# Kernel tuning notes

Measured on AMD Instinct MI355X. Metric: run time of the kernel, lower is better.

## Reference

```python
import jax, jax.numpy as jnp
import numpy as np

B, C, H, W = 2, 72, 96, 96
FACTOR = 4  # input_dim // output_dim = 72 // 18


def setup_inputs() -> dict:
    key = jax.random.key(0)
    ks = jax.random.split(key, 7)
    s = 1.0 / np.sqrt(C)
    return {
        "x": jax.random.normal(ks[0], (B, C, H, W), dtype=jnp.float32),
        "Wq": jax.random.normal(ks[1], (C, C), dtype=jnp.float32) * s,
        "bq": jax.random.normal(ks[2], (C,), dtype=jnp.float32) * 0.01,
        "Wk": jax.random.normal(ks[3], (C, C), dtype=jnp.float32) * s,
        "bk": jax.random.normal(ks[4], (C,), dtype=jnp.float32) * 0.01,
        "Wv": jax.random.normal(ks[5], (C, C), dtype=jnp.float32) * s,
        "bv": jax.random.normal(ks[6], (C,), dtype=jnp.float32) * 0.01,
    }


def reference(x, Wq, bq, Wk, bk, Wv, bv):
    b, c, h, w = x.shape
    n = h * w
    flat = x.reshape(b, c, n)  # [B, C, N]
    # 1x1 convs == per-pixel channel matmuls
    q = jnp.einsum('dc,bcn->bdn', Wq, flat) + bq[None, :, None]
    k = jnp.einsum('dc,bcn->bdn', Wk, flat) + bk[None, :, None]
    v = jnp.einsum('dc,bcn->bdn', Wv, flat) + bv[None, :, None]
    # scores[b,i,j] = sum_c q[b,c,i] * k[b,c,j]  (no 1/sqrt(d) scaling, as in source)
    scores = jnp.einsum('bci,bcj->bij', q, k)  # [B, N, N]
    attn = jax.nn.softmax(scores, axis=-1)
    # weighted_values = bmm(v, attn^T): wv[b,c,i] = sum_j v[b,c,j] * attn[b,i,j]
    wv = jnp.einsum('bcj,bij->bci', v, attn)  # [B, C, N]
    wv = wv.reshape(b, c // FACTOR, FACTOR, h, w)
    xg = x.reshape(b, c // FACTOR, FACTOR, h, w)
    pooled = jnp.sum(xg * wv, axis=2)  # [B, C//FACTOR, H, W]
    return pooled
```

## Files before the change

kernel.cpp:

```cpp
#include <hip/hip_runtime.h>

#define NPIX 9216
#define CIN 72
#define CP 96
#define SPLITS 8
#define JCHUNK (NPIX / SPLITS)
#define JTILES (JCHUNK / 64)
#define L2E   1.44269504088896f
#define EXPB  46.1662413084468f

typedef __attribute__((ext_vector_type(8))) short bf16x8;
typedef __attribute__((ext_vector_type(8))) _Float16 f16x8;
typedef __attribute__((ext_vector_type(4))) float f32x4;

#define MFMA_BF16(A,B,C) __builtin_amdgcn_mfma_f32_16x16x32_bf16(A,B,C,0,0,0)
#define MFMA_F16(A,B,C)  __builtin_amdgcn_mfma_f32_16x16x32_f16(A,B,C,0,0,0)

static __device__ __forceinline__ unsigned short f2bf(float f) {
  unsigned u = __float_as_uint(f);
  u += 0x7fffu + ((u >> 16) & 1u);
  return (unsigned short)(u >> 16);
}
static __device__ __forceinline__ float bf2f(unsigned short h) {
  return __uint_as_float(((unsigned)h) << 16);
}
static __device__ __forceinline__ unsigned short f2h(float f) {
  _Float16 h = (_Float16)f;
  return *(unsigned short*)&h;
}
static __device__ __forceinline__ unsigned pack_bf_trunc(float lo, float hi) {
  return (__float_as_uint(lo) >> 16) | (__float_as_uint(hi) & 0xffff0000u);
}
static __device__ __forceinline__ void load_lds16(const unsigned short* g,
                                                  unsigned short* l) {
  __builtin_amdgcn_global_load_lds(
      (const __attribute__((address_space(1))) unsigned int*)g,
      (__attribute__((address_space(3))) unsigned int*)l, 16, 0, 0);
}

__global__ __launch_bounds__(256) void wprep_kernel(
    const float* __restrict__ Wq, const float* __restrict__ Wk,
    const float* __restrict__ Wv,
    unsigned short* __restrict__ WH, unsigned short* __restrict__ WL)
{
  int id = blockIdx.x * 256 + threadIdx.x;
  if (id >= 3 * 80 * 96) return;
  int mat = id / (80 * 96);
  int rem = id % (80 * 96);
  int d = rem / 96, c = rem % 96;
  const float* W = (mat == 0) ? Wq : (mat == 1) ? Wk : Wv;
  float v = (d < 72 && c < 72) ? W[d * 72 + c] : 0.f;
  unsigned short hi = f2bf(v);
  WH[id] = hi;
  WL[id] = f2bf(v - bf2f(hi));
}

#define XTS 104

__global__ __launch_bounds__(192) void qkv_kernel(
    const float* __restrict__ x,
    const unsigned short* __restrict__ WH, const unsigned short* __restrict__ WL,
    const float* __restrict__ bq, const float* __restrict__ bk,
    const float* __restrict__ bv,
    unsigned short* __restrict__ QH, unsigned short* __restrict__ KH,
    unsigned short* __restrict__ VG)
{
  __shared__ __align__(16) unsigned short xth[16 * XTS];
  __shared__ __align__(16) unsigned short xtl[16 * XTS];
  __shared__ __align__(16) unsigned short obuf[2][16 * XTS];

  const int t    = threadIdx.x;
  const int w    = t >> 6;
  const int lane = t & 63;
  const int quad = lane >> 4;
  const int l15  = lane & 15;
  const int bid  = blockIdx.x;
  const int b    = bid / 576;
  const int n0   = (bid % 576) * 16;

  for (int e = t; e < 288; e += 192) {
    int c = e >> 2, f4 = (e & 3) * 4;
    float4 xv = *(const float4*)(x + ((size_t)b * CIN + c) * NPIX + n0 + f4);
    float vv[4] = {xv.x, xv.y, xv.z, xv.w};
#pragma unroll
    for (int k = 0; k < 4; ++k) {
      unsigned short hi = f2bf(vv[k]);
      xth[(f4 + k) * XTS + c] = hi;
      xtl[(f4 + k) * XTS + c] = f2bf(vv[k] - bf2f(hi));
    }
  }
  for (int e = t; e < 24 * 16; e += 192) {
    int c = 72 + (e >> 4), px = e & 15;
    xth[px * XTS + c] = 0;
    xtl[px * XTS + c] = 0;
  }
  __syncthreads();

  bf16x8 xbh[3], xbl[3];
#pragma unroll
  for (int ks = 0; ks < 3; ++ks) {
    int off = l15 * XTS + ks * 32 + quad * 8;
    xbh[ks] = *(const bf16x8*)(xth + off);
    xbl[ks] = *(const bf16x8*)(xtl + off);
  }

  const unsigned short* wh = WH + w * 80 * 96;
  const unsigned short* wl = WL + w * 80 * 96;
  const float* bias = (w == 0) ? bq : (w == 1) ? bk : bv;

  f32x4 acc[5];
#pragma unroll
  for (int dm = 0; dm < 5; ++dm) {
    acc[dm] = (f32x4){0.f, 0.f, 0.f, 0.f};
#pragma unroll
    for (int ks = 0; ks < 3; ++ks) {
      bf16x8 ah = *(const bf16x8*)(wh + (dm * 16 + l15) * 96 + ks * 32 + quad * 8);
      bf16x8 al = *(const bf16x8*)(wl + (dm * 16 + l15) * 96 + ks * 32 + quad * 8);
      acc[dm] = MFMA_BF16(ah, xbh[ks], acc[dm]);
      acc[dm] = MFMA_BF16(ah, xbl[ks], acc[dm]);
      acc[dm] = MFMA_BF16(al, xbh[ks], acc[dm]);
    }
  }

  if (w < 2) {
    unsigned short* ob = obuf[w];
#pragma unroll
    for (int dm = 0; dm < 5; ++dm)
#pragma unroll
      for (int r = 0; r < 4; ++r) {
        int d = dm * 16 + quad * 4 + r;
        float v = acc[dm][r] + (d < 72 ? bias[d] : 0.f);
        ob[l15 * XTS + d] = f2h(v);
      }
    unsigned short* outp = (w == 0) ? QH : KH;
    const size_t obase = ((size_t)b * NPIX + n0) * CP;
    uint4 z; z.x = z.y = z.z = z.w = 0u;
    for (int f = lane; f < 192; f += 64) {
      int row = f / 12, col = f % 12;
      *(uint4*)(outp + obase + (size_t)row * CP + col * 8) =
          (col < 10) ? *(const uint4*)(ob + row * XTS + col * 8) : z;
    }
  } else {
#pragma unroll
    for (int dm = 0; dm < 5; ++dm)
#pragma unroll
      for (int r = 0; r < 4; ++r) {
        int d = dm * 16 + quad * 4 + r;
        float v = (d < 72) ? acc[dm][r] + bias[d] : (d == 72 ? 1.0f : 0.f);
        VG[((size_t)b * 80 + d) * NPIX + n0 + l15] = f2bf(v);
      }
  }
}

#define KSP 96
#define VSP 72
#define PSP 72

__global__ __launch_bounds__(256, 3) void flash_kernel(
    const float* __restrict__ x,
    const unsigned short* __restrict__ QH, const unsigned short* __restrict__ KH,
    const unsigned short* __restrict__ VG,
    float* __restrict__ NUM, float* __restrict__ LPART)
{
  __shared__ __align__(16) unsigned short ls_kh[64 * KSP];
  __shared__ __align__(16) unsigned short ls_vs[80 * VSP];
  __shared__ __align__(16) unsigned short ps[4][48 * PSP];

  const int t    = threadIdx.x;
  const int w    = t >> 6;
  const int lane = t & 63;
  const int quad = lane >> 4;
  const int l15  = lane & 15;

  const int bid  = blockIdx.x;
  const int sp   = bid & 7;
  const int slot = bid >> 3;
  const int b    = slot / 48;
  const int it   = slot % 48;
  const int i0w  = it * 192 + w * 48;

  f16x8 qh[3][3];
#pragma unroll
  for (int mi = 0; mi < 3; ++mi)
#pragma unroll
    for (int ks = 0; ks < 3; ++ks) {
      size_t off = ((size_t)b * NPIX + i0w + mi * 16 + l15) * CP + ks * 32 + quad * 8;
      qh[mi][ks] = *(const f16x8*)(QH + off);
    }

  f32x4 oacc[3][5];
#pragma unroll
  for (int mi = 0; mi < 3; ++mi)
#pragma unroll
    for (int nt = 0; nt < 5; ++nt) oacc[mi][nt] = (f32x4){0.f, 0.f, 0.f, 0.f};

  unsigned short* psw = ps[w];

  const unsigned short* kpg = KH + ((size_t)b * NPIX + sp * JCHUNK) * CP;
  const unsigned short* vpg = VG + (size_t)b * 80 * NPIX + sp * JCHUNK;

  for (int jt = 0; jt < JTILES; ++jt, kpg += 64 * CP, vpg += 64) {
#pragma unroll
    for (int k = 0; k < 3; ++k) {
      int chunk = w + k * 4;
      load_lds16(kpg + chunk * 512 + lane * 8, ls_kh + chunk * 512);
    }
    for (int idx = t; idx < 640; idx += 256) {
      int r = idx >> 3, c = idx & 7;
      *(uint4*)(ls_vs + r * VSP + c * 8) =
          *(const uint4*)(vpg + (size_t)r * NPIX + c * 8);
    }
    __syncthreads();

#pragma unroll
    for (int tj = 0; tj < 4; ++tj) {
      f16x8 fkh[3];
#pragma unroll
      for (int ks = 0; ks < 3; ++ks)
        fkh[ks] = *(const f16x8*)(ls_kh + (tj * 16 + l15) * KSP + ks * 32 + quad * 8);
#pragma unroll
      for (int mi = 0; mi < 3; ++mi) {
        f32x4 s = (f32x4){0.f, 0.f, 0.f, 0.f};
        s = MFMA_F16(fkh[0], qh[mi][0], s);
        s = MFMA_F16(fkh[1], qh[mi][1], s);
        s = MFMA_F16(fkh[2], qh[mi][2], s);
        float p0 = __builtin_amdgcn_exp2f(__builtin_fmaf(s[0], L2E, -EXPB));
        float p1 = __builtin_amdgcn_exp2f(__builtin_fmaf(s[1], L2E, -EXPB));
        float p2 = __builtin_amdgcn_exp2f(__builtin_fmaf(s[2], L2E, -EXPB));
        float p3 = __builtin_amdgcn_exp2f(__builtin_fmaf(s[3], L2E, -EXPB));
        uint2 pk;
        pk.x = pack_bf_trunc(p0, p1);
        pk.y = pack_bf_trunc(p2, p3);
        *(uint2*)(psw + (mi * 16 + l15) * PSP + tj * 16 + quad * 4) = pk;
      }
    }

#pragma unroll
    for (int js = 0; js < 2; ++js) {
      bf16x8 pf[3];
#pragma unroll
      for (int mi = 0; mi < 3; ++mi)
        pf[mi] = *(const bf16x8*)(psw + (mi * 16 + l15) * PSP + js * 32 + quad * 8);
#pragma unroll
      for (int nt = 0; nt < 5; ++nt) {
        bf16x8 vf = *(const bf16x8*)(ls_vs + (nt * 16 + l15) * VSP + js * 32 + quad * 8);
#pragma unroll
        for (int mi = 0; mi < 3; ++mi)
          oacc[mi][nt] = MFMA_BF16(vf, pf[mi], oacc[mi][nt]);
      }
    }
    __syncthreads();
  }

  const size_t sb = (size_t)(sp * 2 + b);
#pragma unroll
  for (int mi = 0; mi < 3; ++mi) {
    const int i = i0w + mi * 16 + l15;
    if (quad == 2)
      LPART[sb * NPIX + i] = oacc[mi][4][0];
#pragma unroll
    for (int nt = 0; nt < 5; ++nt) {
      int c0 = nt * 16 + quad * 4;
      if (c0 < 72) {
        float num = 0.f;
#pragma unroll
        for (int r = 0; r < 4; ++r)
          num = __builtin_fmaf(x[((size_t)b * CIN + c0 + r) * NPIX + i],
                               oacc[mi][nt][r], num);
        NUM[(sb * 18 + (c0 >> 2)) * NPIX + i] = num;
      }
    }
  }
}

__global__ __launch_bounds__(256) void combine_pool_kernel(
    const float* __restrict__ NUM, const float* __restrict__ LPART,
    float* __restrict__ out)
{
  int id = blockIdx.x * 256 + threadIdx.x;
  if (id >= 2 * 18 * (NPIX / 4)) return;
  int n = (id % (NPIX / 4)) * 4;
  int rest = id / (NPIX / 4);
  int g = rest % 18, b = rest / 18;

  float4 A = make_float4(0.f, 0.f, 0.f, 0.f);
  float4 L = make_float4(0.f, 0.f, 0.f, 0.f);
#pragma unroll
  for (int s = 0; s < SPLITS; ++s) {
    size_t sb = (size_t)(s * 2 + b);
    float4 a = *(const float4*)(NUM + (sb * 18 + g) * NPIX + n);
    float4 l = *(const float4*)(LPART + sb * NPIX + n);
    A.x += a.x; A.y += a.y; A.z += a.z; A.w += a.w;
    L.x += l.x; L.y += l.y; L.z += l.z; L.w += l.w;
  }
  float4 r;
  r.x = A.x / L.x; r.y = A.y / L.y; r.z = A.z / L.z; r.w = A.w / L.w;
  *(float4*)(out + (size_t)id * 4) = r;
}

extern "C" void kernel_launch(void* const* d_in, const int* in_sizes, int n_in,
                              void* d_out, int out_size, void* d_ws, size_t ws_size,
                              hipStream_t stream) {
  const float* x  = (const float*)d_in[0];
  const float* Wq = (const float*)d_in[1];
  const float* bq = (const float*)d_in[2];
  const float* Wk = (const float*)d_in[3];
  const float* bk = (const float*)d_in[4];
  const float* Wv = (const float*)d_in[5];
  const float* bv = (const float*)d_in[6];
  float* out = (float*)d_out;

  char* p = (char*)d_ws;
  const size_t szQK = (size_t)2 * NPIX * CP * 2;
  unsigned short* QH = (unsigned short*)p; p += szQK;
  unsigned short* KH = (unsigned short*)p; p += szQK;
  unsigned short* VG = (unsigned short*)p; p += (size_t)2 * 80 * NPIX * 2;
  unsigned short* WH = (unsigned short*)p; p += (size_t)3 * 80 * 96 * 2;
  unsigned short* WL = (unsigned short*)p; p += (size_t)3 * 80 * 96 * 2;
  float* NUM = (float*)p; p += (size_t)SPLITS * 2 * 18 * NPIX * 4;
  float* LPART = (float*)p; p += (size_t)SPLITS * 2 * NPIX * 4;

  wprep_kernel<<<(3 * 80 * 96 + 255) / 256, 256, 0, stream>>>(Wq, Wk, Wv, WH, WL);
  qkv_kernel<<<1152, 192, 0, stream>>>(x, WH, WL, bq, bk, bv, QH, KH, VG);
  flash_kernel<<<768, 256, 0, stream>>>(x, QH, KH, VG, NUM, LPART);
  combine_pool_kernel<<<(2 * 18 * (NPIX / 4) + 255) / 256, 256, 0, stream>>>(
      NUM, LPART, out);
}
```

Measured before the change: 149.7 us.

## Double-buffer V tile and overlap next-tile loads with second PV half

Double-buffers the V tile in LDS and splits each 64-key tile into two halves. The P·V MFMAs for the first half run before the barrier. The loads of the next K and V tile are then issued before the second-half P·V MFMAs, so global-to-LDS traffic overlaps with matrix work instead of sitting behind a barrier. The per-warp P staging buffer is halved because only 32 columns are live at a time. LDS use stays about the same, but the loop reordering adds some scheduling complexity.

```diff
diff --git a/kernel.cpp b/kernel.cpp
--- a/kernel.cpp
+++ b/kernel.cpp
@@ -154,7 +154,7 @@
 
 #define KSP 96
 #define VSP 72
-#define PSP 72
+#define PSP 36
 
 __global__ __launch_bounds__(256, 3) void flash_kernel(
     const float* __restrict__ x,
@@ -163,7 +163,7 @@
     float* __restrict__ NUM, float* __restrict__ LPART)
 {
   __shared__ __align__(16) unsigned short ls_kh[64 * KSP];
-  __shared__ __align__(16) unsigned short ls_vs[80 * VSP];
+  __shared__ __align__(16) unsigned short ls_vs[2][80 * VSP];
   __shared__ __align__(16) unsigned short ps[4][48 * PSP];
 
   const int t    = threadIdx.x;
@@ -196,60 +196,95 @@
 
   unsigned short* psw = ps[w];
 
-  const unsigned short* kpg = KH + ((size_t)b * NPIX + sp * JCHUNK) * CP;
-  const unsigned short* vpg = VG + (size_t)b * 80 * NPIX + sp * JCHUNK;
-
-  for (int jt = 0; jt < JTILES; ++jt, kpg += 64 * CP, vpg += 64) {
-#pragma unroll
-    for (int k = 0; k < 3; ++k) {
-      int chunk = w + k * 4;
-      load_lds16(kpg + chunk * 512 + lane * 8, ls_kh + chunk * 512);
-    }
-    for (int idx = t; idx < 640; idx += 256) {
-      int r = idx >> 3, c = idx & 7;
-      *(uint4*)(ls_vs + r * VSP + c * 8) =
-          *(const uint4*)(vpg + (size_t)r * NPIX + c * 8);
-    }
+  const unsigned short* kbase = KH + ((size_t)b * NPIX + sp * JCHUNK) * CP;
+  const unsigned short* vbase = VG + (size_t)b * 80 * NPIX + sp * JCHUNK;
+
+#pragma unroll
+  for (int k = 0; k < 3; ++k) {
+    int chunk = w + k * 4;
+    load_lds16(kbase + chunk * 512 + lane * 8, ls_kh + chunk * 512);
+  }
+  for (int idx = t; idx < 640; idx += 256) {
+    int r = idx >> 3, c = idx & 7;
+    *(uint4*)(ls_vs[0] + r * VSP + c * 8) =
+        *(const uint4*)(vbase + (size_t)r * NPIX + c * 8);
+  }
+
+  for (int jt = 0; jt < JTILES; ++jt) {
     __syncthreads();
-
-#pragma unroll
-    for (int tj = 0; tj < 4; ++tj) {
-      f16x8 fkh[3];
-#pragma unroll
-      for (int ks = 0; ks < 3; ++ks)
-        fkh[ks] = *(const f16x8*)(ls_kh + (tj * 16 + l15) * KSP + ks * 32 + quad * 8);
-#pragma unroll
-      for (int mi = 0; mi < 3; ++mi) {
-        f32x4 s = (f32x4){0.f, 0.f, 0.f, 0.f};
-        s = MFMA_F16(fkh[0], qh[mi][0], s);
-        s = MFMA_F16(fkh[1], qh[mi][1], s);
-        s = MFMA_F16(fkh[2], qh[mi][2], s);
-        float p0 = __builtin_amdgcn_exp2f(__builtin_fmaf(s[0], L2E, -EXPB));
-        float p1 = __builtin_amdgcn_exp2f(__builtin_fmaf(s[1], L2E, -EXPB));
-        float p2 = __builtin_amdgcn_exp2f(__builtin_fmaf(s[2], L2E, -EXPB));
-        float p3 = __builtin_amdgcn_exp2f(__builtin_fmaf(s[3], L2E, -EXPB));
-        uint2 pk;
-        pk.x = pack_bf_trunc(p0, p1);
-        pk.y = pack_bf_trunc(p2, p3);
-        *(uint2*)(psw + (mi * 16 + l15) * PSP + tj * 16 + quad * 4) = pk;
-      }
-    }
-
-#pragma unroll
-    for (int js = 0; js < 2; ++js) {
+    const unsigned short* vcur = ls_vs[jt & 1];
+
+#pragma unroll
+    for (int half = 0; half < 2; ++half) {
+#pragma unroll
+      for (int tjh = 0; tjh < 2; ++tjh) {
+        int tj = half * 2 + tjh;
+        f16x8 fkh[3];
+#pragma unroll
+        for (int ks = 0; ks < 3; ++ks)
+          fkh[ks] = *(const f16x8*)(ls_kh + (tj * 16 + l15) * KSP + ks * 32 + quad * 8);
+#pragma unroll
+        for (int mi = 0; mi < 3; ++mi) {
+          f32x4 s = (f32x4){0.f, 0.f, 0.f, 0.f};
+          s = MFMA_F16(fkh[0], qh[mi][0], s);
+          s = MFMA_F16(fkh[1], qh[mi][1], s);
+          s = MFMA_F16(fkh[2], qh[mi][2], s);
+          float p0 = __builtin_amdgcn_exp2f(__builtin_fmaf(s[0], L2E, -EXPB));
+          float p1 = __builtin_amdgcn_exp2f(__builtin_fmaf(s[1], L2E, -EXPB));
+          float p2 = __builtin_amdgcn_exp2f(__builtin_fmaf(s[2], L2E, -EXPB));
+          float p3 = __builtin_amdgcn_exp2f(__builtin_fmaf(s[3], L2E, -EXPB));
+          uint2 pk;
+          pk.x = pack_bf_trunc(p0, p1);
+          pk.y = pack_bf_trunc(p2, p3);
+          *(uint2*)(psw + (mi * 16 + l15) * PSP + tjh * 16 + quad * 4) = pk;
+        }
+      }
+      if (half == 0) {
+        bf16x8 pf[3];
+#pragma unroll
+        for (int mi = 0; mi < 3; ++mi)
+          pf[mi] = *(const bf16x8*)(psw + (mi * 16 + l15) * PSP + quad * 8);
+#pragma unroll
+        for (int nt = 0; nt < 5; ++nt) {
+          bf16x8 vf = *(const bf16x8*)(vcur + (nt * 16 + l15) * VSP + quad * 8);
+#pragma unroll
+          for (int mi = 0; mi < 3; ++mi)
+            oacc[mi][nt] = MFMA_BF16(vf, pf[mi], oacc[mi][nt]);
+        }
+      }
+    }
+
+    __syncthreads();
+
+    if (jt + 1 < JTILES) {
+      const unsigned short* kpg = kbase + (size_t)(jt + 1) * 64 * CP;
+      const unsigned short* vpg = vbase + (jt + 1) * 64;
+      unsigned short* vdst = ls_vs[(jt + 1) & 1];
+#pragma unroll
+      for (int k = 0; k < 3; ++k) {
+        int chunk = w + k * 4;
+        load_lds16(kpg + chunk * 512 + lane * 8, ls_kh + chunk * 512);
+      }
+      for (int idx = t; idx < 640; idx += 256) {
+        int r = idx >> 3, c = idx & 7;
+        *(uint4*)(vdst + r * VSP + c * 8) =
+            *(const uint4*)(vpg + (size_t)r * NPIX + c * 8);
+      }
+    }
+
+    {
       bf16x8 pf[3];
 #pragma unroll
       for (int mi = 0; mi < 3; ++mi)
-        pf[mi] = *(const bf16x8*)(psw + (mi * 16 + l15) * PSP + js * 32 + quad * 8);
+        pf[mi] = *(const bf16x8*)(psw + (mi * 16 + l15) * PSP + quad * 8);
 #pragma unroll
       for (int nt = 0; nt < 5; ++nt) {
-        bf16x8 vf = *(const bf16x8*)(ls_vs + (nt * 16 + l15) * VSP + js * 32 + quad * 8);
+        bf16x8 vf = *(const bf16x8*)(vcur + (nt * 16 + l15) * VSP + 32 + quad * 8);
 #pragma unroll
         for (int mi = 0; mi < 3; ++mi)
           oacc[mi][nt] = MFMA_BF16(vf, pf[mi], oacc[mi][nt]);
       }
     }
-    __syncthreads();
   }
 
   const size_t sb = (size_t)(sp * 2 + b);
```

After: 173.6 us. 16.0% more time.
